# Optimization experiments

Measured on AMD Instinct MI355X. Metric: run time of the kernel, lower is better.

The kernel has to match this reference:

```python
import jax, jax.numpy as jnp
import numpy as np


def setup_inputs() -> dict:
    key = jax.random.key(0)
    k1, k2 = jax.random.split(key)
    N, H, K, E = 8192, 4096, 2, 64
    x = jax.random.normal(k1, (N, H), dtype=jnp.float32)
    row_idx = jnp.arange(N * K, dtype=jnp.int32).reshape(N, K)
    expert_idx = jax.random.randint(k2, (N, K), 0, E, dtype=jnp.int32)
    return {"x": x, "row_idx": row_idx, "expert_idx": expert_idx, "active_num": N * K}


def reference(x, row_idx, expert_idx, active_num):
    # x: [N, H]; row_idx, expert_idx: [N, K]
    N, H = x.shape
    K = expert_idx.shape[1]
    NK = N * K

    expert_flat = expert_idx.reshape(-1)  # [N*K]
    row_flat = row_idx.reshape(-1)        # [N*K]

    # Step 1: stable sort by expert id, carry row indices
    sorted_indices = jnp.argsort(expert_flat, stable=True)
    expanded_expert_idx = expert_flat[sorted_indices]
    dst_to_src = row_flat[sorted_indices]

    # Step 2: invert the permutation: src_to_dst[dst_to_src[i]] = i
    expanded_row_idx = jnp.zeros(NK, dtype=jnp.int32).at[dst_to_src].set(
        jnp.arange(NK, dtype=jnp.int32)
    )

    # Step 3: gather x rows; dst_to_src % N gives the original token row
    expanded_x = x[dst_to_src % N]  # [N*K, H]

    return expanded_x, expanded_row_idx, expanded_expert_idx
```

## Files before the change

### kernel.cpp

```cpp
#include <hip/hip_runtime.h>
#include <hip/hip_bf16.h>

#define TPB 256
#define NEXPERT 64

typedef float f32x4 __attribute__((ext_vector_type(4)));


__global__ void k_hist(const int* __restrict__ expert, int NK, int NB,
                       int* __restrict__ counts) {
    __shared__ int h[NEXPERT];
    const int b = blockIdx.x;
    for (int e = threadIdx.x; e < NEXPERT; e += blockDim.x) h[e] = 0;
    __syncthreads();
    const int i = b * TPB + threadIdx.x;
    if (i < NK) atomicAdd(&h[expert[i]], 1);
    __syncthreads();
    for (int e = threadIdx.x; e < NEXPERT; e += blockDim.x)
        counts[e * NB + b] = h[e];
}

__global__ __launch_bounds__(TPB) void k_scatter(
    const int* __restrict__ expert, const int* __restrict__ rowi,
    int NK, int NB, const int* __restrict__ counts,
    float* __restrict__ out_row, float* __restrict__ out_expert,
    int* __restrict__ dst_of_r) {
    extern __shared__ int lds[];
    __shared__ int h[TPB / 64][NEXPERT + 1];
    const int M = NEXPERT * NB;
    int* cnt = lds;
    int* s = lds + M;
    const int b = blockIdx.x;
    const int tid = threadIdx.x;
    const int w = tid >> 6;
    const int lane = tid & 63;

    for (int j = tid; j < M; j += TPB) cnt[j] = counts[j];
    for (int idx = tid; idx < (TPB / 64) * (NEXPERT + 1); idx += TPB)
        (&h[0][0])[idx] = 0;
    __syncthreads();

    const int ipt = M / TPB;
    const int base_i = tid * ipt;
    int sum = 0;
    for (int j = 0; j < ipt; ++j) sum += cnt[base_i + j];
    s[tid] = sum;
    __syncthreads();
    for (int off = 1; off < TPB; off <<= 1) {
        const int xv = (tid >= off) ? s[tid - off] : 0;
        __syncthreads();
        s[tid] += xv;
        __syncthreads();
    }
    int run = (tid == 0) ? 0 : s[tid - 1];
    for (int j = 0; j < ipt; ++j) {
        const int c = cnt[base_i + j];
        cnt[base_i + j] = run;
        run += c;
    }
    __syncthreads();

    const int i = b * TPB + tid;
    const bool valid = (i < NK);
    const int e = valid ? expert[i] : NEXPERT;

    unsigned long long mask = ~0ull;
#pragma unroll
    for (int bit = 0; bit < 7; ++bit) {
        const unsigned long long bv = __ballot((e >> bit) & 1);
        mask &= ((e >> bit) & 1) ? bv : ~bv;
    }
    const int rank_w = __popcll(mask & ((1ull << lane) - 1ull));
    const int cnt_w  = __popcll(mask);
    if (rank_w == 0) h[w][e] = cnt_w;
    __syncthreads();

    if (valid) {
        int rank = rank_w;
        for (int w2 = 0; w2 < w; ++w2) rank += h[w2][e];
        const int dst = cnt[e * NB + b] + rank;
        const int r = rowi[i];
        out_expert[dst] = (float)e;
        out_row[r] = (float)dst;
        dst_of_r[r] = dst;
    }
}

template <int K>
__global__ void k_gatherT(const float* __restrict__ x,
                          const int* __restrict__ dst_of_r,
                          float* __restrict__ out_x, int H, int N) {
    const int t = blockIdx.x;
    const f32x4* __restrict__ src = (const f32x4*)(x + (size_t)t * (size_t)H);
    size_t ob[K];
#pragma unroll
    for (int kk = 0; kk < K; ++kk)
        ob[kk] = (size_t)dst_of_r[t + kk * N] * (size_t)H;
    const int n4 = H >> 2;
    for (int j = threadIdx.x; j < n4; j += blockDim.x) {
        const f32x4 v = src[j];
#pragma unroll
        for (int kk = 0; kk < K; ++kk)
            __builtin_nontemporal_store(v, (f32x4*)(out_x + ob[kk]) + j);
    }
}

__global__ void k_gather_gen(const float* __restrict__ x,
                             const int* __restrict__ dst_of_r,
                             float* __restrict__ out_x, int H, int N, int K) {
    const int t = blockIdx.x;
    const f32x4* __restrict__ src = (const f32x4*)(x + (size_t)t * (size_t)H);
    const int n4 = H >> 2;
    for (int kk = 0; kk < K; ++kk) {
        const size_t ob = (size_t)dst_of_r[t + kk * N] * (size_t)H;
        for (int j = threadIdx.x; j < n4; j += blockDim.x)
            __builtin_nontemporal_store(src[j], (f32x4*)(out_x + ob) + j);
    }
}

extern "C" void kernel_launch(void* const* d_in, const int* in_sizes, int n_in,
                              void* d_out, int out_size, void* d_ws, size_t ws_size,
                              hipStream_t stream) {
    const float* x    = (const float*)d_in[0];
    const int*   rowi = (const int*)d_in[1];
    const int*   expi = (const int*)d_in[2];

    const int NK = in_sizes[1];
    const int H  = (out_size - 2 * NK) / NK;
    const int N  = in_sizes[0] / H;
    const int K  = NK / N;
    const int NB = (NK + TPB - 1) / TPB;

    float* out_x      = (float*)d_out;
    float* out_row    = out_x + (size_t)NK * (size_t)H;
    float* out_expert = out_row + NK;

    int* counts   = (int*)d_ws;
    int* dst_of_r = counts + NEXPERT * NB;

    const int M = NEXPERT * NB;
    const size_t lds_bytes = (size_t)(M + TPB) * sizeof(int);

    k_hist   <<<NB, TPB, 0, stream>>>(expi, NK, NB, counts);
    k_scatter<<<NB, TPB, lds_bytes, stream>>>(expi, rowi, NK, NB, counts,
                                              out_row, out_expert, dst_of_r);

    switch (K) {
        case 1: k_gatherT<1><<<N, TPB, 0, stream>>>(x, dst_of_r, out_x, H, N); break;
        case 2: k_gatherT<2><<<N, TPB, 0, stream>>>(x, dst_of_r, out_x, H, N); break;
        case 3: k_gatherT<3><<<N, TPB, 0, stream>>>(x, dst_of_r, out_x, H, N); break;
        case 4: k_gatherT<4><<<N, TPB, 0, stream>>>(x, dst_of_r, out_x, H, N); break;
        default: k_gather_gen<<<N, TPB, 0, stream>>>(x, dst_of_r, out_x, H, N, K); break;
    }
}
```

Measured before the change: 75.39 us.

## Fuse histogram and scatter into one kernel with a grid-wide atomic barrier

Merges the per-block expert histogram and the prefix-sum/scatter kernels into a single launch, using a global atomic counter as a grid barrier (with a spin guard) when the block count is at most 256. This is meant to remove one kernel launch and its inter-kernel gap, at the cost of a memset launch and the assumption that all blocks are co-resident. It also makes the prefix-sum loop bounds-safe when M is not a multiple of TPB.

```diff
diff --git a/kernel.cpp b/kernel.cpp
--- a/kernel.cpp
+++ b/kernel.cpp
@@ -6,6 +6,93 @@
 
 typedef float f32x4 __attribute__((ext_vector_type(4)));
 
+__global__ __launch_bounds__(TPB) void k_prelude_bar(
+    const int* __restrict__ expert, const int* __restrict__ rowi,
+    int NK, int NB, unsigned* __restrict__ bar, int* __restrict__ counts,
+    float* __restrict__ out_row, float* __restrict__ out_expert,
+    int* __restrict__ dst_of_r) {
+    extern __shared__ int lds[];
+    __shared__ int h64[NEXPERT];
+    __shared__ int hw[TPB / 64][NEXPERT + 1];
+    const int M = NEXPERT * NB;
+    int* cnt = lds;
+    int* s = lds + M;
+    const int b = blockIdx.x;
+    const int tid = threadIdx.x;
+    const int w = tid >> 6;
+    const int lane = tid & 63;
+
+    if (tid < NEXPERT) h64[tid] = 0;
+    __syncthreads();
+    const int i = b * TPB + tid;
+    const bool valid = (i < NK);
+    const int e = valid ? expert[i] : NEXPERT;
+    if (valid) atomicAdd(&h64[e], 1);
+    __syncthreads();
+    if (tid < NEXPERT) counts[tid * NB + b] = h64[tid];
+
+    __threadfence();
+    __syncthreads();
+    if (tid == 0) {
+        __hip_atomic_fetch_add(bar, 1u, __ATOMIC_ACQ_REL,
+                               __HIP_MEMORY_SCOPE_AGENT);
+        long long guard = 0;
+        while (__hip_atomic_load(bar, __ATOMIC_ACQUIRE,
+                                 __HIP_MEMORY_SCOPE_AGENT) < (unsigned)NB) {
+            __builtin_amdgcn_s_sleep(2);
+            if (++guard > (1LL << 22)) break;
+        }
+    }
+    __syncthreads();
+
+    for (int j = tid; j < M; j += TPB) cnt[j] = counts[j];
+    for (int idx = tid; idx < (TPB / 64) * (NEXPERT + 1); idx += TPB)
+        (&hw[0][0])[idx] = 0;
+    __syncthreads();
+
+    const int ipt = (M + TPB - 1) / TPB;
+    const int base_i = tid * ipt;
+    int sum = 0;
+    for (int j = 0; j < ipt; ++j) sum += (base_i + j < M) ? cnt[base_i + j] : 0;
+    s[tid] = sum;
+    __syncthreads();
+    for (int off = 1; off < TPB; off <<= 1) {
+        const int xv = (tid >= off) ? s[tid - off] : 0;
+        __syncthreads();
+        s[tid] += xv;
+        __syncthreads();
+    }
+    int run = (tid == 0) ? 0 : s[tid - 1];
+    for (int j = 0; j < ipt; ++j) {
+        if (base_i + j < M) {
+            const int c = cnt[base_i + j];
+            cnt[base_i + j] = run;
+            run += c;
+        }
+    }
+    __syncthreads();
+
+    unsigned long long mask = ~0ull;
+#pragma unroll
+    for (int bit = 0; bit < 7; ++bit) {
+        const unsigned long long bv = __ballot((e >> bit) & 1);
+        mask &= ((e >> bit) & 1) ? bv : ~bv;
+    }
+    const int rank_w = __popcll(mask & ((1ull << lane) - 1ull));
+    const int cnt_w  = __popcll(mask);
+    if (rank_w == 0) hw[w][e] = cnt_w;
+    __syncthreads();
+
+    if (valid) {
+        int rank = rank_w;
+        for (int w2 = 0; w2 < w; ++w2) rank += hw[w2][e];
+        const int dst = cnt[e * NB + b] + rank;
+        const int r = rowi[i];
+        out_expert[dst] = (float)e;
+        out_row[r] = (float)dst;
+        dst_of_r[r] = dst;
+    }
+}
 
 __global__ void k_hist(const int* __restrict__ expert, int NK, int NB,
                        int* __restrict__ counts) {
@@ -40,10 +127,10 @@
         (&h[0][0])[idx] = 0;
     __syncthreads();
 
-    const int ipt = M / TPB;
+    const int ipt = (M + TPB - 1) / TPB;
     const int base_i = tid * ipt;
     int sum = 0;
-    for (int j = 0; j < ipt; ++j) sum += cnt[base_i + j];
+    for (int j = 0; j < ipt; ++j) sum += (base_i + j < M) ? cnt[base_i + j] : 0;
     s[tid] = sum;
     __syncthreads();
     for (int off = 1; off < TPB; off <<= 1) {
@@ -54,9 +141,11 @@
     }
     int run = (tid == 0) ? 0 : s[tid - 1];
     for (int j = 0; j < ipt; ++j) {
-        const int c = cnt[base_i + j];
-        cnt[base_i + j] = run;
-        run += c;
+        if (base_i + j < M) {
+            const int c = cnt[base_i + j];
+            cnt[base_i + j] = run;
+            run += c;
+        }
     }
     __syncthreads();
 
@@ -135,15 +224,22 @@
     float* out_row    = out_x + (size_t)NK * (size_t)H;
     float* out_expert = out_row + NK;
 
-    int* counts   = (int*)d_ws;
+    unsigned* bar = (unsigned*)d_ws;
+    int* counts   = (int*)d_ws + 64;
     int* dst_of_r = counts + NEXPERT * NB;
 
     const int M = NEXPERT * NB;
     const size_t lds_bytes = (size_t)(M + TPB) * sizeof(int);
 
-    k_hist   <<<NB, TPB, 0, stream>>>(expi, NK, NB, counts);
-    k_scatter<<<NB, TPB, lds_bytes, stream>>>(expi, rowi, NK, NB, counts,
-                                              out_row, out_expert, dst_of_r);
+    if (NB <= 256) {
+        hipMemsetAsync(bar, 0, sizeof(unsigned), stream);
+        k_prelude_bar<<<NB, TPB, lds_bytes, stream>>>(
+            expi, rowi, NK, NB, bar, counts, out_row, out_expert, dst_of_r);
+    } else {
+        k_hist   <<<NB, TPB, 0, stream>>>(expi, NK, NB, counts);
+        k_scatter<<<NB, TPB, lds_bytes, stream>>>(expi, rowi, NK, NB, counts,
+                                                  out_row, out_expert, dst_of_r);
+    }
 
     switch (K) {
         case 1: k_gatherT<1><<<N, TPB, 0, stream>>>(x, dst_of_r, out_x, H, N); break;
```

Result: slower. 83.85 us (+11.2%).
